# Kernel optimization log

Hardware: AMD Instinct MI355X
Metric: run time of the kernel (lower is better)

## Reference

```python
import jax, jax.numpy as jnp
import numpy as np

N_NODES = 100000
N_EDGES = 1600000
IN_FEATS = 128
N_HIDDEN = 32
N_CLASSES = 47
HEADS = (4, 4)
NEG_SLOPE = 0.2


def setup_inputs() -> dict:
    key = jax.random.key(0)
    ks = jax.random.split(key, 12)
    x = jax.random.normal(ks[0], (N_NODES, IN_FEATS), dtype=jnp.float32)
    src = jax.random.randint(ks[1], (N_EDGES,), 0, N_NODES)
    dst = jax.random.randint(ks[2], (N_EDGES,), 0, N_NODES)
    inverse_idx = jax.random.randint(ks[3], (N_NODES,), 0, N_NODES)
    h1 = HEADS[0] * N_HIDDEN
    s1 = 1.0 / np.sqrt(IN_FEATS)
    W1 = jax.random.normal(ks[4], (IN_FEATS, h1), dtype=jnp.float32) * s1
    al1 = jax.random.normal(ks[5], (HEADS[0], N_HIDDEN), dtype=jnp.float32) * 0.1
    ar1 = jax.random.normal(ks[6], (HEADS[0], N_HIDDEN), dtype=jnp.float32) * 0.1
    b1 = jnp.zeros((h1,), dtype=jnp.float32)
    h2 = HEADS[1] * N_CLASSES
    s2 = 1.0 / np.sqrt(h1)
    W2 = jax.random.normal(ks[7], (h1, h2), dtype=jnp.float32) * s2
    al2 = jax.random.normal(ks[8], (HEADS[1], N_CLASSES), dtype=jnp.float32) * 0.1
    ar2 = jax.random.normal(ks[9], (HEADS[1], N_CLASSES), dtype=jnp.float32) * 0.1
    b2 = jnp.zeros((h2,), dtype=jnp.float32)
    return {"x": x, "src": src, "dst": dst, "inverse_idx": inverse_idx,
            "W1": W1, "al1": al1, "ar1": ar1, "b1": b1,
            "W2": W2, "al2": al2, "ar2": ar2, "b2": b2}


def gat_conv(h, src, dst, W, al, ar, b, heads, out_dim, apply_elu):
    # DGL GATConv (feat_drop=attn_drop=0, eval mode):
    # projected per-head features, edge attention, per-dst softmax, aggregate.
    feat = (h @ W).reshape(-1, heads, out_dim)               # (N, H, D)
    el = jnp.einsum('nhd,hd->nh', feat, al)                  # (N, H)
    er = jnp.einsum('nhd,hd->nh', feat, ar)                  # (N, H)
    e = el[src] + er[dst]                                    # (E, H)
    e = jnp.where(e > 0, e, NEG_SLOPE * e)                   # LeakyReLU
    m = jax.ops.segment_max(e, dst, num_segments=N_NODES)    # (N, H)
    m = jnp.where(jnp.isfinite(m), m, 0.0)
    ex = jnp.exp(e - m[dst])
    s = jax.ops.segment_sum(ex, dst, num_segments=N_NODES)   # (N, H)
    alpha = ex / jnp.maximum(s[dst], 1e-9)                   # (E, H)
    msg = feat[src] * alpha[:, :, None]                      # (E, H, D)
    out = jax.ops.segment_sum(msg, dst, num_segments=N_NODES)  # (N, H, D)
    out = out + b.reshape(1, heads, out_dim)
    if apply_elu:
        out = jax.nn.elu(out)
    return out


def reference(x, src, dst, inverse_idx, W1, al1, ar1, b1, W2, al2, ar2, b2):
    # Layer 0: GATConv + ELU, flatten heads, then NPFeatureShuffle reindex.
    h = gat_conv(x, src, dst, W1, al1, ar1, b1, HEADS[0], N_HIDDEN, True)
    h = h.reshape(N_NODES, HEADS[0] * N_HIDDEN)
    h = h[inverse_idx]  # cross-partition shuffle reindex
    # Layer 1: GATConv, no activation, mean over heads.
    h = gat_conv(h, src, dst, W2, al2, ar2, b2, HEADS[1], N_CLASSES, False)
    return h.mean(axis=1)  # (N, n_classes)
```

## Files before the change

### kernel.cpp

```cpp
#include <hip/hip_runtime.h>
#include <hip/hip_bf16.h>
#include <hip/hip_fp16.h>
#include <type_traits>

#define N_NODES 100000
#define N_EDGES 1600000

typedef _Float16 half8_t __attribute__((ext_vector_type(8)));
typedef _Float16 half4_t __attribute__((ext_vector_type(4)));
typedef float floatx4 __attribute__((ext_vector_type(4)));

__global__ void csr_prep(const int* __restrict__ dst, int* __restrict__ deg, int E,
                         const float* __restrict__ W1, const float* __restrict__ W2,
                         const float* __restrict__ al1, const float* __restrict__ ar1,
                         const float* __restrict__ al2, const float* __restrict__ ar2,
                         __half* __restrict__ Wt1, __half* __restrict__ Wt2) {
    const int b = blockIdx.x;
    if (b < 6250) {
        int i = b * 256 + threadIdx.x;
        if (i < E) atomicAdd(&deg[dst[i]], 1);
        return;
    }
    const int c = b - 6250;
    const int k = threadIdx.x;
    if (k >= 128) return;
    if (c < 128) {
        Wt1[c * 128 + k] = __float2half(W1[k * 128 + c]);
    } else if (c < 144) {
        int j = c - 128;
        float v = 0.f;
        if (j < 8) {
            int h = j & 3;
            const float* a = (j < 4) ? al1 : ar1;
            for (int d = 0; d < 32; ++d)
                v = fmaf(W1[k * 128 + h * 32 + d], a[h * 32 + d], v);
        }
        Wt1[c * 128 + k] = __float2half(v);
    } else if (c < 336) {
        int c2 = c - 144;
        float v = (c2 < 188) ? W2[k * 188 + c2] : 0.f;
        Wt2[c2 * 128 + k] = __float2half(v);
    } else {
        int j = c - 336;
        float v = 0.f;
        if (j < 8) {
            int h = j & 3;
            const float* a = (j < 4) ? al2 : ar2;
            for (int d = 0; d < 47; ++d)
                v = fmaf(W2[k * 188 + h * 47 + d], a[h * 47 + d], v);
        }
        Wt2[(192 + j) * 128 + k] = __float2half(v);
    }
}

__global__ void block_sums(const int* __restrict__ deg, int* __restrict__ bsum, int N) {
    __shared__ int ws[4];
    const int t = threadIdx.x;
    int i = blockIdx.x * 256 + t;
    int v = (i < N) ? deg[i] : 0;
    #pragma unroll
    for (int o = 32; o; o >>= 1) v += __shfl_down(v, o, 64);
    if ((t & 63) == 0) ws[t >> 6] = v;
    __syncthreads();
    if (t == 0) bsum[blockIdx.x] = ws[0] + ws[1] + ws[2] + ws[3];
}

__global__ void scan_bsum(int* __restrict__ bsum, int nb) {
    __shared__ int sh[512];
    const int t = threadIdx.x;
    sh[t] = (t < nb) ? bsum[t] : 0;
    __syncthreads();
    for (int o = 1; o < 512; o <<= 1) {
        int v = (t >= o) ? sh[t - o] : 0;
        __syncthreads();
        sh[t] += v;
        __syncthreads();
    }
    if (t < nb) bsum[t] = sh[t];
}

__global__ void scan_final(const int* __restrict__ deg, const int* __restrict__ bsum,
                           int* __restrict__ row_ptr, int* __restrict__ cursor, int N) {
    __shared__ int ws[4];
    const int t = threadIdx.x;
    const int b = blockIdx.x;
    const int i = b * 256 + t;
    const int lane = t & 63;
    const int wid = t >> 6;
    int v = (i < N) ? deg[i] : 0;
    int x = v;
    #pragma unroll
    for (int o = 1; o < 64; o <<= 1) {
        int y = __shfl_up(x, o, 64);
        if (lane >= o) x += y;
    }
    if (lane == 63) ws[wid] = x;
    __syncthreads();
    int prefix = (b > 0) ? bsum[b - 1] : 0;
    for (int k = 0; k < wid; ++k) prefix += ws[k];
    if (i < N) {
        row_ptr[i + 1] = prefix + x;
        cursor[i] = prefix + x - v;
    }
    if (i == 0) row_ptr[0] = 0;
}

template <int TT, int NLOG, int OSTRIDE, bool EMBED, bool GATHER, typename AT>
__device__ __forceinline__ void gemm_body(
    int bx,
    const AT* __restrict__ A, const __half* __restrict__ Wt,
    __half* __restrict__ C, __half* __restrict__ elh, float* __restrict__ er,
    const int* __restrict__ gather, int N) {
    constexpr int LDA = 136;
    __shared__ _Float16 As[64 * LDA];
    __shared__ int ridx[64];
    const int tid = threadIdx.x;
    const int r0 = bx * 64;

    if (tid < 64) {
        int row = r0 + tid;
        int pr = 0;
        if (row < N) pr = GATHER ? gather[row] : row;
        ridx[tid] = pr;
    }
    __syncthreads();

    {
        const int r = tid >> 2, q = tid & 3;
        const int src = ridx[r];
        if constexpr (std::is_same<AT, float>::value) {
            const float4* A4 = (const float4*)A;
            #pragma unroll
            for (int i = 0; i < 8; ++i) {
                float4 v = A4[(size_t)src * 32 + q * 8 + i];
                half4_t hv = {(_Float16)v.x, (_Float16)v.y, (_Float16)v.z, (_Float16)v.w};
                *(half4_t*)&As[r * LDA + q * 32 + i * 4] = hv;
            }
        } else {
            const uint4* A4 = (const uint4*)A;
            #pragma unroll
            for (int i = 0; i < 4; ++i) {
                uint4 v = A4[(size_t)src * 16 + q * 4 + i];
                *(uint4*)&As[r * LDA + q * 32 + i * 8] = v;
            }
        }
    }
    __syncthreads();

    const int lane = tid & 63;
    const int wave = tid >> 6;
    const int col = lane & 15;
    const int quad = lane >> 4;
    const int arow = wave * 16 + col;

    floatx4 acc[TT];
    #pragma unroll
    for (int t = 0; t < TT; ++t) acc[t] = (floatx4){0.f, 0.f, 0.f, 0.f};

    #pragma unroll
    for (int kc = 0; kc < 4; ++kc) {
        half8_t a = *(const half8_t*)&As[arow * LDA + kc * 32 + quad * 8];
        #pragma unroll
        for (int t = 0; t < TT; ++t) {
            half8_t b = *(const half8_t*)&Wt[(size_t)(t * 16 + col) * 128 + kc * 32 + quad * 8];
            acc[t] = __builtin_amdgcn_mfma_f32_16x16x32_f16(a, b, acc[t], 0, 0, 0);
        }
    }

    #pragma unroll
    for (int t = 0; t < TT - 1; ++t) {
        #pragma unroll
        for (int r = 0; r < 4; ++r) {
            int row = r0 + wave * 16 + quad * 4 + r;
            int c = t * 16 + col;
            if (row < N && c < NLOG) {
                int sc = EMBED ? (c + c / 47) : c;
                C[(size_t)row * OSTRIDE + sc] = __float2half(acc[t][r]);
            }
        }
    }
    #pragma unroll
    for (int r = 0; r < 4; ++r) {
        int row = r0 + wave * 16 + quad * 4 + r;
        if (row < N) {
            if (col < 4) {
                if constexpr (EMBED)
                    C[(size_t)row * OSTRIDE + col * 48 + 47] = __float2half(acc[TT - 1][r]);
                else
                    elh[row * 4 + col] = __float2half(acc[TT - 1][r]);
            } else if (col < 8) {
                er[row * 4 + (col - 4)] = acc[TT - 1][r];
            }
        }
    }
}

template <int TT, int NLOG, int OSTRIDE, bool EMBED, bool GATHER, typename AT>
__global__ __launch_bounds__(256) void gemm_mfma(
    const AT* __restrict__ A, const __half* __restrict__ Wt,
    __half* __restrict__ C, __half* __restrict__ elh, float* __restrict__ er,
    const int* __restrict__ gather, int N) {
    gemm_body<TT, NLOG, OSTRIDE, EMBED, GATHER, AT>(blockIdx.x, A, Wt, C, elh, er, gather, N);
}

__global__ __launch_bounds__(256) void scatter_gemm1(
    const int* __restrict__ src, const int* __restrict__ dst,
    int* __restrict__ cursor, int* __restrict__ e_src, int E,
    const float* __restrict__ A, const __half* __restrict__ Wt,
    __half* __restrict__ C, __half* __restrict__ elh, float* __restrict__ er, int N) {
    const int g = blockIdx.x >> 3;
    if ((g & 1) == 0) {
        const int part = blockIdx.x & 7;
        const int sb = g >> 1;
        const int psz = N_NODES / 8;
        const int lo = part * psz;
        const int hi = lo + psz;
        const int SLICE = E / 200;
        const int4* d4 = (const int4*)(dst + sb * SLICE);
        const int4* s4 = (const int4*)(src + sb * SLICE);
        const int nvec = SLICE / 4;
        for (int v = threadIdx.x; v < nvec; v += 256) {
            int4 dd = d4[v];
            int4 ss = s4[v];
            if (dd.x >= lo && dd.x < hi) e_src[atomicAdd(&cursor[dd.x], 1)] = ss.x;
            if (dd.y >= lo && dd.y < hi) e_src[atomicAdd(&cursor[dd.y], 1)] = ss.y;
            if (dd.z >= lo && dd.z < hi) e_src[atomicAdd(&cursor[dd.z], 1)] = ss.z;
            if (dd.w >= lo && dd.w < hi) e_src[atomicAdd(&cursor[dd.w], 1)] = ss.w;
        }
    } else {
        const int bx = (g >> 1) * 8 + (blockIdx.x & 7);
        if (bx * 64 < N)
            gemm_body<9, 128, 128, false, false, float>(bx, A, Wt, C, elh, er, nullptr, N);
    }
}

__global__ __launch_bounds__(256) void gat_gather1(
    const __half* __restrict__ feat, const __half* __restrict__ elh,
    const float* __restrict__ er,
    const int* __restrict__ row_ptr, const int* __restrict__ e_src,
    const float* __restrict__ bias, __half* __restrict__ out) {
    const int t = threadIdx.x;
    const int lane = t & 63;
    const int n = blockIdx.x * 4 + (t >> 6);
    const int h = lane >> 4;
    const int start = row_ptr[n], end = row_ptr[n + 1];
    const char* fb = (const char*)feat;
    const uint32_t flo = (uint32_t)lane * 4u;
    const float ern = er[n * 4 + h];
    float ax = 0.f, ay = 0.f, s = 0.f;
    int i = start;
    for (; i + 4 <= end; i += 4) {
        int sv0 = e_src[i + 0], sv1 = e_src[i + 1], sv2 = e_src[i + 2], sv3 = e_src[i + 3];
        float e0 = __half2float(elh[sv0 * 4 + h]) + ern;
        float e1 = __half2float(elh[sv1 * 4 + h]) + ern;
        float e2 = __half2float(elh[sv2 * 4 + h]) + ern;
        float e3 = __half2float(elh[sv3 * 4 + h]) + ern;
        float w0 = __expf(fmaxf(e0, 0.2f * e0));
        float w1 = __expf(fmaxf(e1, 0.2f * e1));
        float w2 = __expf(fmaxf(e2, 0.2f * e2));
        float w3 = __expf(fmaxf(e3, 0.2f * e3));
        __half2 f0 = *(const __half2*)(fb + (uint32_t)sv0 * 256u + flo);
        __half2 f1 = *(const __half2*)(fb + (uint32_t)sv1 * 256u + flo);
        __half2 f2v = *(const __half2*)(fb + (uint32_t)sv2 * 256u + flo);
        __half2 f3 = *(const __half2*)(fb + (uint32_t)sv3 * 256u + flo);
        float2 g0 = __half22float2(f0), g1 = __half22float2(f1);
        float2 g2 = __half22float2(f2v), g3 = __half22float2(f3);
        s += (w0 + w1) + (w2 + w3);
        ax += w0 * g0.x + w1 * g1.x + w2 * g2.x + w3 * g3.x;
        ay += w0 * g0.y + w1 * g1.y + w2 * g2.y + w3 * g3.y;
    }
    for (; i < end; ++i) {
        int sv = e_src[i];
        float e = __half2float(elh[sv * 4 + h]) + ern;
        float ww = __expf(fmaxf(e, 0.2f * e));
        float2 g = __half22float2(*(const __half2*)(fb + (uint32_t)sv * 256u + flo));
        s += ww;
        ax += ww * g.x;
        ay += ww * g.y;
    }
    float inv = 1.f / fmaxf(s, 1e-9f);
    float ox = ax * inv + bias[lane * 2 + 0];
    float oy = ay * inv + bias[lane * 2 + 1];
    ox = (ox > 0.f) ? ox : (__expf(ox) - 1.f);
    oy = (oy > 0.f) ? oy : (__expf(oy) - 1.f);
    ((__half2*)out)[(size_t)n * 64 + lane] = __floats2half2_rn(ox, oy);
}

__global__ __launch_bounds__(256) void gat_gather2(
    const __half* __restrict__ feat, const float* __restrict__ er,
    const int* __restrict__ row_ptr, const int* __restrict__ e_src,
    const float* __restrict__ bias, float* __restrict__ out) {
    const int t = threadIdx.x;
    const int lane = t & 63;
    const int n = blockIdx.x * 4 + (t >> 6);
    if (lane < 48) {
        const int h = lane / 12;
        const int q = lane - h * 12;
        const int g11 = h * 12 + 11;
        const int start = row_ptr[n], end = row_ptr[n + 1];
        const char* fb = (const char*)feat;
        const uint32_t flo = (uint32_t)lane * 8u;
        const float ern = er[n * 4 + h];
        float a0 = 0.f, a1 = 0.f, a2 = 0.f, a3 = 0.f, s = 0.f;
        int i = start;
        for (; i + 4 <= end; i += 4) {
            int sv0 = e_src[i + 0], sv1 = e_src[i + 1], sv2 = e_src[i + 2], sv3 = e_src[i + 3];
            half4_t f0 = *(const half4_t*)(fb + (uint32_t)sv0 * 384u + flo);
            half4_t f1 = *(const half4_t*)(fb + (uint32_t)sv1 * 384u + flo);
            half4_t f2 = *(const half4_t*)(fb + (uint32_t)sv2 * 384u + flo);
            half4_t f3 = *(const half4_t*)(fb + (uint32_t)sv3 * 384u + flo);
            float e0 = __shfl((float)f0[3], g11, 64) + ern;
            float e1 = __shfl((float)f1[3], g11, 64) + ern;
            float e2 = __shfl((float)f2[3], g11, 64) + ern;
            float e3 = __shfl((float)f3[3], g11, 64) + ern;
            float w0 = __expf(fmaxf(e0, 0.2f * e0));
            float w1 = __expf(fmaxf(e1, 0.2f * e1));
            float w2 = __expf(fmaxf(e2, 0.2f * e2));
            float w3 = __expf(fmaxf(e3, 0.2f * e3));
            s += (w0 + w1) + (w2 + w3);
            a0 += w0 * (float)f0[0] + w1 * (float)f1[0] + w2 * (float)f2[0] + w3 * (float)f3[0];
            a1 += w0 * (float)f0[1] + w1 * (float)f1[1] + w2 * (float)f2[1] + w3 * (float)f3[1];
            a2 += w0 * (float)f0[2] + w1 * (float)f1[2] + w2 * (float)f2[2] + w3 * (float)f3[2];
            a3 += w0 * (float)f0[3] + w1 * (float)f1[3] + w2 * (float)f2[3] + w3 * (float)f3[3];
        }
        for (; i < end; ++i) {
            int sv = e_src[i];
            half4_t f0 = *(const half4_t*)(fb + (uint32_t)sv * 384u + flo);
            float e = __shfl((float)f0[3], g11, 64) + ern;
            float ww = __expf(fmaxf(e, 0.2f * e));
            s += ww;
            a0 += ww * (float)f0[0];
            a1 += ww * (float)f0[1];
            a2 += ww * (float)f0[2];
            a3 += ww * (float)f0[3];
        }
        if (q == 11) a3 = 0.f;
        float inv = 1.f / fmaxf(s, 1e-9f);
        const int d0 = q * 4;
        float b0 = bias[h * 47 + d0 + 0];
        float b1 = bias[h * 47 + d0 + 1];
        float b2 = bias[h * 47 + d0 + 2];
        float b3 = (d0 + 3 < 47) ? bias[h * 47 + d0 + 3] : 0.f;
        float r0 = a0 * inv + b0;
        float r1 = a1 * inv + b1;
        float r2 = a2 * inv + b2;
        float r3 = a3 * inv + b3;
        float t0 = r0 + __shfl(r0, lane + 12, 64) + __shfl(r0, lane + 24, 64) + __shfl(r0, lane + 36, 64);
        float t1 = r1 + __shfl(r1, lane + 12, 64) + __shfl(r1, lane + 24, 64) + __shfl(r1, lane + 36, 64);
        float t2 = r2 + __shfl(r2, lane + 12, 64) + __shfl(r2, lane + 24, 64) + __shfl(r2, lane + 36, 64);
        float t3 = r3 + __shfl(r3, lane + 12, 64) + __shfl(r3, lane + 24, 64) + __shfl(r3, lane + 36, 64);
        if (h == 0) {
            size_t base = (size_t)n * 47 + d0;
            out[base + 0] = 0.25f * t0;
            out[base + 1] = 0.25f * t1;
            out[base + 2] = 0.25f * t2;
            if (d0 + 3 < 47) out[base + 3] = 0.25f * t3;
        }
    }
}

extern "C" void kernel_launch(void* const* d_in, const int* in_sizes, int n_in,
                              void* d_out, int out_size, void* d_ws, size_t ws_size,
                              hipStream_t stream) {
    const int N = N_NODES, E = N_EDGES;
    const float* x    = (const float*)d_in[0];
    const int*   src  = (const int*)d_in[1];
    const int*   dst  = (const int*)d_in[2];
    const int*   inv  = (const int*)d_in[3];
    const float* W1   = (const float*)d_in[4];
    const float* al1  = (const float*)d_in[5];
    const float* ar1  = (const float*)d_in[6];
    const float* b1   = (const float*)d_in[7];
    const float* W2   = (const float*)d_in[8];
    const float* al2  = (const float*)d_in[9];
    const float* ar2  = (const float*)d_in[10];
    const float* b2   = (const float*)d_in[11];
    float* out = (float*)d_out;

    char* p = (char*)d_ws;
    auto carve = [&](size_t bytes) {
        char* q = p;
        p += (bytes + 255) & ~size_t(255);
        return q;
    };
    __half* feat1   = (__half*)carve((size_t)N * 128 * 2);
    __half* feat2   = (__half*)carve((size_t)N * 192 * 2);
    __half* hbuf    = (__half*)carve((size_t)N * 128 * 2);
    __half* Wt1     = (__half*)carve(144 * 128 * 2);
    __half* Wt2     = (__half*)carve(208 * 128 * 2);
    __half* elh1    = (__half*)carve((size_t)N * 4 * 2);
    float*  er      = (float*)carve((size_t)N * 4 * 4);
    int*    deg     = (int*)carve((size_t)N * 4);
    int*    row_ptr = (int*)carve((size_t)(N + 1) * 4);
    int*    cursor  = (int*)carve((size_t)N * 4);
    int*    bsum    = (int*)carve(512 * 4);
    int*    e_src   = (int*)carve((size_t)E * 4);

    const int nb = (N + 255) / 256;

    hipMemsetAsync(deg, 0, (size_t)N * 4, stream);
    csr_prep<<<6250 + 352, 256, 0, stream>>>(dst, deg, E, W1, W2, al1, ar1, al2, ar2, Wt1, Wt2);
    block_sums<<<nb, 256, 0, stream>>>(deg, bsum, N);
    scan_bsum<<<1, 512, 0, stream>>>(bsum, nb);
    scan_final<<<nb, 256, 0, stream>>>(deg, bsum, row_ptr, cursor, N);

    scatter_gemm1<<<3200, 256, 0, stream>>>(src, dst, cursor, e_src, E,
                                            x, Wt1, feat1, elh1, er, N);

    gat_gather1<<<(N + 3) / 4, 256, 0, stream>>>(feat1, elh1, er, row_ptr, e_src, b1, hbuf);

    gemm_mfma<13, 188, 192, true, true, __half><<<(N + 63) / 64, 256, 0, stream>>>(
        hbuf, Wt2, feat2, nullptr, er, inv, N);
    gat_gather2<<<(N + 3) / 4, 256, 0, stream>>>(feat2, er, row_ptr, e_src, b2, out);
}
```

Baseline: 495.8 us.

## Split fused scatter/GEMM kernel, unroll gathers by 8, fold log2e into attention weights

Separates the fused edge-scatter plus layer-1 GEMM kernel into two launches, undoing the co-scheduling of atomics-bound and MFMA work. Adds an 8-way unrolled edge loop to both gather kernels so more independent feature loads are in flight. Prescales the attention projection columns by log2(e) so exp2f can replace __expf in the softmax. Splitting removes the overlap between scatter and GEMM and adds a launch, while the unrolling raises register pressure.

```diff
diff --git a/kernel.cpp b/kernel.cpp
--- a/kernel.cpp
+++ b/kernel.cpp
@@ -5,6 +5,7 @@
 
 #define N_NODES 100000
 #define N_EDGES 1600000
+#define LOG2E 1.44269504f
 
 typedef _Float16 half8_t __attribute__((ext_vector_type(8)));
 typedef _Float16 half4_t __attribute__((ext_vector_type(4)));
@@ -35,7 +36,7 @@
             for (int d = 0; d < 32; ++d)
                 v = fmaf(W1[k * 128 + h * 32 + d], a[h * 32 + d], v);
         }
-        Wt1[c * 128 + k] = __float2half(v);
+        Wt1[c * 128 + k] = __float2half(v * LOG2E);
     } else if (c < 336) {
         int c2 = c - 144;
         float v = (c2 < 188) ? W2[k * 188 + c2] : 0.f;
@@ -49,7 +50,7 @@
             for (int d = 0; d < 47; ++d)
                 v = fmaf(W2[k * 188 + h * 47 + d], a[h * 47 + d], v);
         }
-        Wt2[(192 + j) * 128 + k] = __float2half(v);
+        Wt2[(192 + j) * 128 + k] = __float2half(v * LOG2E);
     }
 }
 
@@ -105,9 +106,30 @@
     if (i == 0) row_ptr[0] = 0;
 }
 
+__global__ __launch_bounds__(256) void scatter_edges_part(
+    const int* __restrict__ src, const int* __restrict__ dst,
+    int* __restrict__ cursor, int* __restrict__ e_src, int E) {
+    const int part = blockIdx.x & 7;
+    const int sb = blockIdx.x >> 3;
+    const int psz = N_NODES / 8;
+    const int lo = part * psz;
+    const int hi = lo + psz;
+    const int SLICE = E / 200;
+    const int4* d4 = (const int4*)(dst + sb * SLICE);
+    const int4* s4 = (const int4*)(src + sb * SLICE);
+    const int nvec = SLICE / 4;
+    for (int v = threadIdx.x; v < nvec; v += 256) {
+        int4 dd = d4[v];
+        int4 ss = s4[v];
+        if (dd.x >= lo && dd.x < hi) e_src[atomicAdd(&cursor[dd.x], 1)] = ss.x;
+        if (dd.y >= lo && dd.y < hi) e_src[atomicAdd(&cursor[dd.y], 1)] = ss.y;
+        if (dd.z >= lo && dd.z < hi) e_src[atomicAdd(&cursor[dd.z], 1)] = ss.z;
+        if (dd.w >= lo && dd.w < hi) e_src[atomicAdd(&cursor[dd.w], 1)] = ss.w;
+    }
+}
+
 template <int TT, int NLOG, int OSTRIDE, bool EMBED, bool GATHER, typename AT>
-__device__ __forceinline__ void gemm_body(
-    int bx,
+__global__ __launch_bounds__(256) void gemm_mfma(
     const AT* __restrict__ A, const __half* __restrict__ Wt,
     __half* __restrict__ C, __half* __restrict__ elh, float* __restrict__ er,
     const int* __restrict__ gather, int N) {
@@ -115,7 +137,7 @@
     __shared__ _Float16 As[64 * LDA];
     __shared__ int ridx[64];
     const int tid = threadIdx.x;
-    const int r0 = bx * 64;
+    const int r0 = blockIdx.x * 64;
 
     if (tid < 64) {
         int row = r0 + tid;
@@ -195,45 +217,6 @@
     }
 }
 
-template <int TT, int NLOG, int OSTRIDE, bool EMBED, bool GATHER, typename AT>
-__global__ __launch_bounds__(256) void gemm_mfma(
-    const AT* __restrict__ A, const __half* __restrict__ Wt,
-    __half* __restrict__ C, __half* __restrict__ elh, float* __restrict__ er,
-    const int* __restrict__ gather, int N) {
-    gemm_body<TT, NLOG, OSTRIDE, EMBED, GATHER, AT>(blockIdx.x, A, Wt, C, elh, er, gather, N);
-}
-
-__global__ __launch_bounds__(256) void scatter_gemm1(
-    const int* __restrict__ src, const int* __restrict__ dst,
-    int* __restrict__ cursor, int* __restrict__ e_src, int E,
-    const float* __restrict__ A, const __half* __restrict__ Wt,
-    __half* __restrict__ C, __half* __restrict__ elh, float* __restrict__ er, int N) {
-    const int g = blockIdx.x >> 3;
-    if ((g & 1) == 0) {
-        const int part = blockIdx.x & 7;
-        const int sb = g >> 1;
-        const int psz = N_NODES / 8;
-        const int lo = part * psz;
-        const int hi = lo + psz;
-        const int SLICE = E / 200;
-        const int4* d4 = (const int4*)(dst + sb * SLICE);
-        const int4* s4 = (const int4*)(src + sb * SLICE);
-        const int nvec = SLICE / 4;
-        for (int v = threadIdx.x; v < nvec; v += 256) {
-            int4 dd = d4[v];
-            int4 ss = s4[v];
-            if (dd.x >= lo && dd.x < hi) e_src[atomicAdd(&cursor[dd.x], 1)] = ss.x;
-            if (dd.y >= lo && dd.y < hi) e_src[atomicAdd(&cursor[dd.y], 1)] = ss.y;
-            if (dd.z >= lo && dd.z < hi) e_src[atomicAdd(&cursor[dd.z], 1)] = ss.z;
-            if (dd.w >= lo && dd.w < hi) e_src[atomicAdd(&cursor[dd.w], 1)] = ss.w;
-        }
-    } else {
-        const int bx = (g >> 1) * 8 + (blockIdx.x & 7);
-        if (bx * 64 < N)
-            gemm_body<9, 128, 128, false, false, float>(bx, A, Wt, C, elh, er, nullptr, N);
-    }
-}
-
 __global__ __launch_bounds__(256) void gat_gather1(
     const __half* __restrict__ feat, const __half* __restrict__ elh,
     const float* __restrict__ er,
@@ -249,16 +232,53 @@
     const float ern = er[n * 4 + h];
     float ax = 0.f, ay = 0.f, s = 0.f;
     int i = start;
+    for (; i + 8 <= end; i += 8) {
+        int sv0 = e_src[i + 0], sv1 = e_src[i + 1], sv2 = e_src[i + 2], sv3 = e_src[i + 3];
+        int sv4 = e_src[i + 4], sv5 = e_src[i + 5], sv6 = e_src[i + 6], sv7 = e_src[i + 7];
+        __half2 f0 = *(const __half2*)(fb + (uint32_t)sv0 * 256u + flo);
+        __half2 f1 = *(const __half2*)(fb + (uint32_t)sv1 * 256u + flo);
+        __half2 f2v = *(const __half2*)(fb + (uint32_t)sv2 * 256u + flo);
+        __half2 f3 = *(const __half2*)(fb + (uint32_t)sv3 * 256u + flo);
+        __half2 f4 = *(const __half2*)(fb + (uint32_t)sv4 * 256u + flo);
+        __half2 f5 = *(const __half2*)(fb + (uint32_t)sv5 * 256u + flo);
+        __half2 f6 = *(const __half2*)(fb + (uint32_t)sv6 * 256u + flo);
+        __half2 f7 = *(const __half2*)(fb + (uint32_t)sv7 * 256u + flo);
+        float e0 = __half2float(elh[sv0 * 4 + h]) + ern;
+        float e1 = __half2float(elh[sv1 * 4 + h]) + ern;
+        float e2 = __half2float(elh[sv2 * 4 + h]) + ern;
+        float e3 = __half2float(elh[sv3 * 4 + h]) + ern;
+        float e4 = __half2float(elh[sv4 * 4 + h]) + ern;
+        float e5 = __half2float(elh[sv5 * 4 + h]) + ern;
+        float e6 = __half2float(elh[sv6 * 4 + h]) + ern;
+        float e7 = __half2float(elh[sv7 * 4 + h]) + ern;
+        float w0 = exp2f(fmaxf(e0, 0.2f * e0));
+        float w1 = exp2f(fmaxf(e1, 0.2f * e1));
+        float w2 = exp2f(fmaxf(e2, 0.2f * e2));
+        float w3 = exp2f(fmaxf(e3, 0.2f * e3));
+        float w4 = exp2f(fmaxf(e4, 0.2f * e4));
+        float w5 = exp2f(fmaxf(e5, 0.2f * e5));
+        float w6 = exp2f(fmaxf(e6, 0.2f * e6));
+        float w7 = exp2f(fmaxf(e7, 0.2f * e7));
+        float2 g0 = __half22float2(f0), g1 = __half22float2(f1);
+        float2 g2 = __half22float2(f2v), g3 = __half22float2(f3);
+        float2 g4 = __half22float2(f4), g5 = __half22float2(f5);
+        float2 g6 = __half22float2(f6), g7 = __half22float2(f7);
+        s += ((w0 + w1) + (w2 + w3)) + ((w4 + w5) + (w6 + w7));
+        ax += (w0 * g0.x + w1 * g1.x + w2 * g2.x + w3 * g3.x)
+            + (w4 * g4.x + w5 * g5.x + w6 * g6.x + w7 * g7.x);
+        ay += (w0 * g0.y + w1 * g1.y + w2 * g2.y + w3 * g3.y)
+            + (w4 * g4.y + w5 * g5.y + w6 * g6.y + w7 * g7.y);
+    }
     for (; i + 4 <= end; i += 4) {
         int sv0 = e_src[i + 0], sv1 = e_src[i + 1], sv2 = e_src[i + 2], sv3 = e_src[i + 3];
         float e0 = __half2float(elh[sv0 * 4 + h]) + ern;
         float e1 = __half2float(elh[sv1 * 4 + h]) + ern;
         float e2 = __half2float(elh[sv2 * 4 + h]) + ern;
         float e3 = __half2float(elh[sv3 * 4 + h]) + ern;
-        float w0 = __expf(fmaxf(e0, 0.2f * e0));
-        float w1 = __expf(fmaxf(e1, 0.2f * e1));
-        float w2 = __expf(fmaxf(e2, 0.2f * e2));
-        float w3 = __expf(fmaxf(e3, 0.2f * e3));
+        float w0 = exp2f(fmaxf(e0, 0.2f * e0));
+        float w1 = exp2f(fmaxf(e1, 0.2f * e1));
+        float w2 = exp2f(fmaxf(e2, 0.2f * e2));
+        float w3 = exp2f(fmaxf(e3, 0.2f * e3));
         __half2 f0 = *(const __half2*)(fb + (uint32_t)sv0 * 256u + flo);
         __half2 f1 = *(const __half2*)(fb + (uint32_t)sv1 * 256u + flo);
         __half2 f2v = *(const __half2*)(fb + (uint32_t)sv2 * 256u + flo);
@@ -272,7 +292,7 @@
     for (; i < end; ++i) {
         int sv = e_src[i];
         float e = __half2float(elh[sv * 4 + h]) + ern;
-        float ww = __expf(fmaxf(e, 0.2f * e));
+        float ww = exp2f(fmaxf(e, 0.2f * e));
         float2 g = __half22float2(*(const __half2*)(fb + (uint32_t)sv * 256u + flo));
         s += ww;
         ax += ww * g.x;
@@ -303,6 +323,43 @@
         const float ern = er[n * 4 + h];
         float a0 = 0.f, a1 = 0.f, a2 = 0.f, a3 = 0.f, s = 0.f;
         int i = start;
+        for (; i + 8 <= end; i += 8) {
+            int sv0 = e_src[i + 0], sv1 = e_src[i + 1], sv2 = e_src[i + 2], sv3 = e_src[i + 3];
+            int sv4 = e_src[i + 4], sv5 = e_src[i + 5], sv6 = e_src[i + 6], sv7 = e_src[i + 7];
+            half4_t f0 = *(const half4_t*)(fb + (uint32_t)sv0 * 384u + flo);
+            half4_t f1 = *(const half4_t*)(fb + (uint32_t)sv1 * 384u + flo);
+            half4_t f2 = *(const half4_t*)(fb + (uint32_t)sv2 * 384u + flo);
+            half4_t f3 = *(const half4_t*)(fb + (uint32_t)sv3 * 384u + flo);
+            half4_t f4 = *(const half4_t*)(fb + (uint32_t)sv4 * 384u + flo);
+            half4_t f5 = *(const half4_t*)(fb + (uint32_t)sv5 * 384u + flo);
+            half4_t f6 = *(const half4_t*)(fb + (uint32_t)sv6 * 384u + flo);
+            half4_t f7 = *(const half4_t*)(fb + (uint32_t)sv7 * 384u + flo);
+            float e0 = __shfl((float)f0[3], g11, 64) + ern;
+            float e1 = __shfl((float)f1[3], g11, 64) + ern;
+            float e2 = __shfl((float)f2[3], g11, 64) + ern;
+            float e3 = __shfl((float)f3[3], g11, 64) + ern;
+            float e4 = __shfl((float)f4[3], g11, 64) + ern;
+            float e5 = __shfl((float)f5[3], g11, 64) + ern;
+            float e6 = __shfl((float)f6[3], g11, 64) + ern;
+            float e7 = __shfl((float)f7[3], g11, 64) + ern;
+            float w0 = exp2f(fmaxf(e0, 0.2f * e0));
+            float w1 = exp2f(fmaxf(e1, 0.2f * e1));
+            float w2 = exp2f(fmaxf(e2, 0.2f * e2));
+            float w3 = exp2f(fmaxf(e3, 0.2f * e3));
+            float w4 = exp2f(fmaxf(e4, 0.2f * e4));
+            float w5 = exp2f(fmaxf(e5, 0.2f * e5));
+            float w6 = exp2f(fmaxf(e6, 0.2f * e6));
+            float w7 = exp2f(fmaxf(e7, 0.2f * e7));
+            s += ((w0 + w1) + (w2 + w3)) + ((w4 + w5) + (w6 + w7));
+            a0 += (w0 * (float)f0[0] + w1 * (float)f1[0] + w2 * (float)f2[0] + w3 * (float)f3[0])
+                + (w4 * (float)f4[0] + w5 * (float)f5[0] + w6 * (float)f6[0] + w7 * (float)f7[0]);
+            a1 += (w0 * (float)f0[1] + w1 * (float)f1[1] + w2 * (float)f2[1] + w3 * (float)f3[1])
+                + (w4 * (float)f4[1] + w5 * (float)f5[1] + w6 * (float)f6[1] + w7 * (float)f7[1]);
+            a2 += (w0 * (float)f0[2] + w1 * (float)f1[2] + w2 * (float)f2[2] + w3 * (float)f3[2])
+                + (w4 * (float)f4[2] + w5 * (float)f5[2] + w6 * (float)f6[2] + w7 * (float)f7[2]);
+            a3 += (w0 * (float)f0[3] + w1 * (float)f1[3] + w2 * (float)f2[3] + w3 * (float)f3[3])
+                + (w4 * (float)f4[3] + w5 * (float)f5[3] + w6 * (float)f6[3] + w7 * (float)f7[3]);
+        }
         for (; i + 4 <= end; i += 4) {
             int sv0 = e_src[i + 0], sv1 = e_src[i + 1], sv2 = e_src[i + 2], sv3 = e_src[i + 3];
             half4_t f0 = *(const half4_t*)(fb + (uint32_t)sv0 * 384u + flo);
@@ -313,10 +370,10 @@
             float e1 = __shfl((float)f1[3], g11, 64) + ern;
             float e2 = __shfl((float)f2[3], g11, 64) + ern;
             float e3 = __shfl((float)f3[3], g11, 64) + ern;
-            float w0 = __expf(fmaxf(e0, 0.2f * e0));
-            float w1 = __expf(fmaxf(e1, 0.2f * e1));
-            float w2 = __expf(fmaxf(e2, 0.2f * e2));
-            float w3 = __expf(fmaxf(e3, 0.2f * e3));
+            float w0 = exp2f(fmaxf(e0, 0.2f * e0));
+            float w1 = exp2f(fmaxf(e1, 0.2f * e1));
+            float w2 = exp2f(fmaxf(e2, 0.2f * e2));
+            float w3 = exp2f(fmaxf(e3, 0.2f * e3));
             s += (w0 + w1) + (w2 + w3);
             a0 += w0 * (float)f0[0] + w1 * (float)f1[0] + w2 * (float)f2[0] + w3 * (float)f3[0];
             a1 += w0 * (float)f0[1] + w1 * (float)f1[1] + w2 * (float)f2[1] + w3 * (float)f3[1];
@@ -327,7 +384,7 @@
             int sv = e_src[i];
             half4_t f0 = *(const half4_t*)(fb + (uint32_t)sv * 384u + flo);
             float e = __shfl((float)f0[3], g11, 64) + ern;
-            float ww = __expf(fmaxf(e, 0.2f * e));
+            float ww = exp2f(fmaxf(e, 0.2f * e));
             s += ww;
             a0 += ww * (float)f0[0];
             a1 += ww * (float)f0[1];
@@ -404,8 +461,10 @@
     scan_bsum<<<1, 512, 0, stream>>>(bsum, nb);
     scan_final<<<nb, 256, 0, stream>>>(deg, bsum, row_ptr, cursor, N);
 
-    scatter_gemm1<<<3200, 256, 0, stream>>>(src, dst, cursor, e_src, E,
-                                            x, Wt1, feat1, elh1, er, N);
+    scatter_edges_part<<<1600, 256, 0, stream>>>(src, dst, cursor, e_src, E);
+
+    gemm_mfma<9, 128, 128, false, false, float><<<(N + 63) / 64, 256, 0, stream>>>(
+        x, Wt1, feat1, elh1, er, nullptr, N);
 
     gat_gather1<<<(N + 3) / 4, 256, 0, stream>>>(feat1, elh1, er, row_ptr, e_src, b1, hbuf);
 
```

After: 521.1 us. 1.05x slower.
